# Kernel tuning notes

Measured on AMD Instinct MI355X. Metric: run time of the kernel, lower is better.

Reference implementation:

```python
import jax, jax.numpy as jnp
import numpy as np


def setup_inputs() -> dict:
    key = jax.random.key(0)
    k1, k2, k3 = jax.random.split(key, 3)
    B, H, L, D = 4, 16, 1024, 64
    q = jax.random.normal(k1, (B, H, L, D), dtype=jnp.float32)
    k = jax.random.normal(k2, (B, H, L, D), dtype=jnp.float32)
    attn_mask = jax.random.randint(k3, (B, H, L, L), 0, 2).astype(bool)
    return {"q": q, "k": k, "attn_mask": attn_mask}


def reference(q, k, attn_mask):
    # q, k: [B, H, L, D]. The original builds a [B,H,L,D,L] tensor
    # c[b,h,i,m,j] = exp(-(q[b,h,i,m]-k[b,h,j,m])^2), then for each dim m
    # keeps only the entries where rank of q[i,m] (along seq) equals rank of
    # k[j,m], scatters them into an LxL grid and averages over m.
    # Equivalent fused form: sort q and k per dimension, pair equal ranks,
    # and scatter-add exp(-(q_sorted - k_sorted)^2)/D into p[b,h,i,j].
    B, H, L, D = q.shape
    q_idx = jnp.argsort(q, axis=2)                       # [B,H,L,D] int
    k_idx = jnp.argsort(k, axis=2)
    q_sorted = jnp.take_along_axis(q, q_idx, axis=2)     # [B,H,L,D]
    k_sorted = jnp.take_along_axis(k, k_idx, axis=2)
    diff = q_sorted - k_sorted
    vals = jnp.exp(-(diff * diff))                       # [B,H,L,D]
    # linear index into the flattened [L,L] grid, plus batch*head offset
    lin = q_idx * L + k_idx                              # [B,H,L,D]
    bh_off = (jnp.arange(B * H) * (L * L)).reshape(B, H, 1, 1)
    flat_idx = (lin + bh_off).ravel()
    p = jnp.zeros(B * H * L * L, dtype=q.dtype).at[flat_idx].add(vals.ravel())
    p = (p / D).reshape(B, H, L, L)
    return jnp.where(attn_mask, jnp.zeros((), dtype=p.dtype), p)
```

## Files before the change

kernel.cpp:

```cpp
#include <hip/hip_runtime.h>
#include <stdint.h>
#include <string.h>


#define LL 1024
#define DD 64
#define NBH 64
#define PAIRS_BYTES ((size_t)NBH * DD * LL * 4)

typedef float    vf4   __attribute__((ext_vector_type(4)));
typedef uint32_t vu4   __attribute__((ext_vector_type(4)));
typedef int32_t  vi4   __attribute__((ext_vector_type(4)));

__device__ __forceinline__ uint32_t f2ord(float x) {
    uint32_t u = __float_as_uint(x);
    return (u & 0x80000000u) ? ~u : (u | 0x80000000u);
}
__device__ __forceinline__ float ord2f(uint32_t o) {
    uint32_t u = (o & 0x80000000u) ? (o & 0x7fffffffu) : ~o;
    return __uint_as_float(u);
}
__device__ __forceinline__ void cex(uint64_t& a, uint64_t& b, bool up) {
    const uint64_t lo = a < b ? a : b;
    const uint64_t hi = a < b ? b : a;
    a = up ? lo : hi; b = up ? hi : lo;
}
__device__ __forceinline__ uint64_t shfl64(uint64_t v, int m) {
    const uint32_t lo = __shfl_xor((uint32_t)v, m);
    const uint32_t hi = __shfl_xor((uint32_t)(v >> 32), m);
    return ((uint64_t)hi << 32) | lo;
}

__device__ __forceinline__ void wave_bitonic16(uint64_t x[16], const int lane) {
    #pragma unroll
    for (int lk = 1; lk <= 3; ++lk) {
        const int k2 = 1 << lk;
        #pragma unroll
        for (int j = k2 >> 1; j >= 1; j >>= 1) {
            #pragma unroll
            for (int s = 0; s < 16; ++s)
                if ((s & j) == 0) cex(x[s], x[s | j], ((s & k2) == 0));
        }
    }
    {
        const bool up = ((lane & 1) == 0);
        #pragma unroll
        for (int j = 8; j >= 1; j >>= 1) {
            #pragma unroll
            for (int s = 0; s < 16; ++s)
                if ((s & j) == 0) cex(x[s], x[s | j], up);
        }
    }
    #pragma unroll
    for (int lk = 5; lk <= 10; ++lk) {
        const bool up = ((lane & (1 << (lk - 4))) == 0);
        #pragma unroll
        for (int m = 1 << (lk - 5); m >= 1; m >>= 1) {
            const bool keepmin = (((lane & m) == 0) == up);
            #pragma unroll
            for (int s = 0; s < 16; ++s) {
                const uint64_t y = shfl64(x[s], m);
                x[s] = keepmin ? (x[s] < y ? x[s] : y)
                               : (x[s] > y ? x[s] : y);
            }
        }
        #pragma unroll
        for (int j = 8; j >= 1; j >>= 1) {
            #pragma unroll
            for (int s = 0; s < 16; ++s)
                if ((s & j) == 0) cex(x[s], x[s | j], up);
        }
    }
}

__global__ __launch_bounds__(256, 3) void swd3_phase1(
    const float* __restrict__ q, const float* __restrict__ k,
    uint32_t* __restrict__ pairs)
{
    __shared__ alignas(16) uint32_t pr[4][LL];

    const int raw  = blockIdx.x;
    const int slot = raw >> 3;
    const int bh   = (raw & 7) * 8 + (slot >> 4);
    const int dg   = slot & 15;
    const int t    = threadIdx.x;
    const int w    = t >> 6;
    const int lane = t & 63;
    const int d    = dg * 4 + w;

    const size_t colbase = (size_t)bh * (LL * DD) + d;

    uint64_t xq[16], xk[16];
    #pragma unroll
    for (int s = 0; s < 16; ++s) {
        const uint32_t e = 16u * (uint32_t)lane + (uint32_t)s;
        xq[s] = ((uint64_t)f2ord(q[colbase + (size_t)e * DD]) << 32) | e;
        xk[s] = ((uint64_t)f2ord(k[colbase + (size_t)e * DD]) << 32) | e;
    }
    wave_bitonic16(xq, lane);
    wave_bitonic16(xk, lane);

    uint32_t* prw = pr[w];
    #pragma unroll
    for (int s = 0; s < 16; ++s) {
        const uint32_t iq = (uint32_t)xq[s] & 1023u;
        const uint32_t ik = (uint32_t)xk[s] & 1023u;
        const float df = ord2f((uint32_t)(xq[s] >> 32))
                       - ord2f((uint32_t)(xk[s] >> 32));
        const float val = __expf(-df * df) * (1.0f / 64.0f);
        prw[iq] = (__float_as_uint(val) & 0xFFFFFC00u) | ik;
    }
    __asm__ volatile("s_waitcnt lgkmcnt(0)" ::: "memory");
    vu4* pp4 = (vu4*)(pairs + ((size_t)bh * DD + d) * LL);
    const vu4* src = (const vu4*)prw;
    #pragma unroll
    for (int r = 0; r < 4; ++r)
        pp4[r * 64 + lane] = src[r * 64 + lane];
}

__global__ __launch_bounds__(256) void swd3_phase2(
    const uint32_t* __restrict__ pairs, const void* __restrict__ maskp,
    float* __restrict__ out)
{
    __shared__ alignas(16) float acc[8 * LL];
    __shared__ uint32_t sdet[4];

    const int bh = blockIdx.x >> 7;
    const int s  = blockIdx.x & 127;
    const int i0 = s * 8;
    const int t  = threadIdx.x;

    {
        const uint32_t w = ((const uint32_t*)maskp)[t];
        const uint64_t bal = __ballot(w > 1u);
        if ((t & 63) == 0) sdet[t >> 6] = (bal != 0ull) ? 1u : 0u;
    }

    vf4* acc4 = (vf4*)acc;
    #pragma unroll
    for (int v = 0; v < 8; ++v) {
        vf4 z; z.x = 0.f; z.y = 0.f; z.z = 0.f; z.w = 0.f;
        acc4[v * 256 + t] = z;
    }
    __syncthreads();

    const bool mask_byte =
        ((sdet[0] | sdet[1] | sdet[2] | sdet[3]) != 0u);
    const size_t cellbase = ((size_t)bh << 20) + ((size_t)i0 << 10);

    uint32_t mb[8];
    vi4      mi[8];
    if (mask_byte) {
        const uint32_t* mp = (const uint32_t*)maskp + (cellbase >> 2);
        #pragma unroll
        for (int v = 0; v < 8; ++v)
            mb[v] = __builtin_nontemporal_load(mp + v * 256 + t);
    } else {
        const vi4* mp = (const vi4*)((const int32_t*)maskp + cellbase);
        #pragma unroll
        for (int v = 0; v < 8; ++v)
            mi[v] = __builtin_nontemporal_load(mp + v * 256 + t);
    }

    {
        const uint32_t* pb = pairs + (size_t)bh * (DD * LL);
        const int dd = t >> 2;
        const uint2 pv = ((const uint2*)(pb + dd * LL + i0))[t & 3];
        const int ii0 = 2 * (t & 3), ii1 = ii0 + 1;
        atomicAdd(&acc[ii0 * LL + (int)(pv.x & 1023u)],
                  __uint_as_float(pv.x & 0xFFFFFC00u));
        atomicAdd(&acc[ii1 * LL + (int)(pv.y & 1023u)],
                  __uint_as_float(pv.y & 0xFFFFFC00u));
    }
    __syncthreads();

    vf4* ob = (vf4*)(out + cellbase);
    #pragma unroll
    for (int v = 0; v < 8; ++v) {
        const int p = v * 256 + t;
        const vf4 a = acc4[p];
        int mx, my, mz, mw2;
        if (mask_byte) {
            const uint32_t m = mb[v];
            mx = (int)(m & 0xFFu); my = (int)((m >> 8) & 0xFFu);
            mz = (int)((m >> 16) & 0xFFu); mw2 = (int)(m >> 24);
        } else {
            mx = mi[v].x; my = mi[v].y; mz = mi[v].z; mw2 = mi[v].w;
        }
        vf4 r;
        r.x = mx  ? 0.f : a.x;
        r.y = my  ? 0.f : a.y;
        r.z = mz  ? 0.f : a.z;
        r.w = mw2 ? 0.f : a.w;
        __builtin_nontemporal_store(r, ob + p);
    }
}

extern "C" void kernel_launch(void* const* d_in, const int* in_sizes, int n_in,
                              void* d_out, int out_size, void* d_ws, size_t ws_size,
                              hipStream_t stream) {
    const float* q = (const float*)d_in[0];
    const float* k = (const float*)d_in[1];
    const void* mask = d_in[2];
    uint32_t* pairs = (uint32_t*)d_ws;

    const bool ws_ok = (ws_size >= PAIRS_BYTES);
    hipError_t e1 = hipSuccess, e2 = hipSuccess;
    (void)hipGetLastError();

    if (ws_ok) {
        swd3_phase1<<<NBH * DD / 4, 256, 0, stream>>>(q, k, pairs);
        swd3_phase1<<<NBH * DD / 4, 256, 0, stream>>>(q, k, pairs);
        e1 = hipGetLastError();
        swd3_phase2<<<NBH * 128, 256, 0, stream>>>(pairs, mask, (float*)d_out);
        e2 = hipGetLastError();
    }

    if (!ws_ok || e1 != hipSuccess || e2 != hipSuccess) {
        static float h_stamp[8];
        h_stamp[0] = !ws_ok ? (9000.0f + (float)(ws_size >> 20))
                            : (1000.0f + (float)(int)e1);
        h_stamp[1] = 2000.0f + (float)(int)e2;
        h_stamp[2] = h_stamp[0];
        h_stamp[3] = h_stamp[1];
        hipMemcpyAsync(d_out, h_stamp, sizeof(h_stamp),
                       hipMemcpyHostToDevice, stream);
    }
}
```

Before: 634.9 us.

## Pre-transpose q/k into column-major workspace and drop the duplicate sort launch

Adds a tiled shared-memory transpose kernel that writes q and k as order-preserving uint32 keys in a per-dimension contiguous layout. This lets the sort kernel read each column with coalesced 16-byte vector loads instead of 256-byte-strided scalar loads. The redundant second launch of the sort kernel is removed. The block index of the scatter/mask kernel is also swizzled to interleave batch-heads. The cost is an extra kernel launch, an extra pass over q and k, and a workspace three times larger; if the workspace is too small, the error-stamp fallback runs instead of the computation.

```diff
diff --git a/kernel.cpp b/kernel.cpp
--- a/kernel.cpp
+++ b/kernel.cpp
@@ -6,7 +6,8 @@
 #define LL 1024
 #define DD 64
 #define NBH 64
-#define PAIRS_BYTES ((size_t)NBH * DD * LL * 4)
+#define MAT_WORDS ((size_t)NBH * DD * LL)
+#define WS_BYTES (3 * MAT_WORDS * 4)
 
 typedef float    vf4   __attribute__((ext_vector_type(4)));
 typedef uint32_t vu4   __attribute__((ext_vector_type(4)));
@@ -73,8 +74,49 @@
     }
 }
 
+__global__ __launch_bounds__(256) void swd3_transpose(
+    const float* __restrict__ q, const float* __restrict__ k,
+    uint32_t* __restrict__ qt, uint32_t* __restrict__ kt)
+{
+    __shared__ uint32_t tq[64][65];
+    __shared__ uint32_t tk[64][65];
+
+    const int b  = blockIdx.x;
+    const int bh = (b & 7) * 8 + ((b >> 3) & 7);
+    const int e0 = (b >> 6) * 64;
+    const int t  = threadIdx.x;
+
+    const size_t base = (size_t)bh * (LL * DD);
+    #pragma unroll
+    for (int i = 0; i < 4; ++i) {
+        const int idx = i * 256 + t;
+        const int r   = idx >> 4;
+        const int c   = (idx & 15) * 4;
+        const vf4 vq = *(const vf4*)(q + base + (size_t)(e0 + r) * DD + c);
+        const vf4 vk = *(const vf4*)(k + base + (size_t)(e0 + r) * DD + c);
+        tq[r][c + 0] = f2ord(vq.x); tq[r][c + 1] = f2ord(vq.y);
+        tq[r][c + 2] = f2ord(vq.z); tq[r][c + 3] = f2ord(vq.w);
+        tk[r][c + 0] = f2ord(vk.x); tk[r][c + 1] = f2ord(vk.y);
+        tk[r][c + 2] = f2ord(vk.z); tk[r][c + 3] = f2ord(vk.w);
+    }
+    __syncthreads();
+    #pragma unroll
+    for (int i = 0; i < 4; ++i) {
+        const int idx = i * 256 + t;
+        const int d   = idx >> 4;
+        const int c   = (idx & 15) * 4;
+        vu4 v;
+        v.x = tq[c + 0][d]; v.y = tq[c + 1][d];
+        v.z = tq[c + 2][d]; v.w = tq[c + 3][d];
+        *(vu4*)(qt + base + (size_t)d * LL + e0 + c) = v;
+        v.x = tk[c + 0][d]; v.y = tk[c + 1][d];
+        v.z = tk[c + 2][d]; v.w = tk[c + 3][d];
+        *(vu4*)(kt + base + (size_t)d * LL + e0 + c) = v;
+    }
+}
+
 __global__ __launch_bounds__(256, 3) void swd3_phase1(
-    const float* __restrict__ q, const float* __restrict__ k,
+    const uint32_t* __restrict__ qt, const uint32_t* __restrict__ kt,
     uint32_t* __restrict__ pairs)
 {
     __shared__ alignas(16) uint32_t pr[4][LL];
@@ -88,14 +130,23 @@
     const int lane = t & 63;
     const int d    = dg * 4 + w;
 
-    const size_t colbase = (size_t)bh * (LL * DD) + d;
+    const uint32_t* colq = qt + (size_t)bh * (DD * LL) + (size_t)d * LL;
+    const uint32_t* colk = kt + (size_t)bh * (DD * LL) + (size_t)d * LL;
 
     uint64_t xq[16], xk[16];
     #pragma unroll
-    for (int s = 0; s < 16; ++s) {
-        const uint32_t e = 16u * (uint32_t)lane + (uint32_t)s;
-        xq[s] = ((uint64_t)f2ord(q[colbase + (size_t)e * DD]) << 32) | e;
-        xk[s] = ((uint64_t)f2ord(k[colbase + (size_t)e * DD]) << 32) | e;
+    for (int r = 0; r < 4; ++r) {
+        const vu4 vq = *(const vu4*)(colq + 256 * r + 4 * lane);
+        const vu4 vk = *(const vu4*)(colk + 256 * r + 4 * lane);
+        const uint32_t eb = 256u * r + 4u * lane;
+        xq[4 * r + 0] = ((uint64_t)vq.x << 32) | (eb + 0);
+        xq[4 * r + 1] = ((uint64_t)vq.y << 32) | (eb + 1);
+        xq[4 * r + 2] = ((uint64_t)vq.z << 32) | (eb + 2);
+        xq[4 * r + 3] = ((uint64_t)vq.w << 32) | (eb + 3);
+        xk[4 * r + 0] = ((uint64_t)vk.x << 32) | (eb + 0);
+        xk[4 * r + 1] = ((uint64_t)vk.y << 32) | (eb + 1);
+        xk[4 * r + 2] = ((uint64_t)vk.z << 32) | (eb + 2);
+        xk[4 * r + 3] = ((uint64_t)vk.w << 32) | (eb + 3);
     }
     wave_bitonic16(xq, lane);
     wave_bitonic16(xk, lane);
@@ -125,9 +176,10 @@
     __shared__ alignas(16) float acc[8 * LL];
     __shared__ uint32_t sdet[4];
 
-    const int bh = blockIdx.x >> 7;
-    const int s  = blockIdx.x & 127;
-    const int i0 = s * 8;
+    const int b  = blockIdx.x;
+    const int bh = (b & 7) * 8 + ((b >> 3) & 7);
+    const int st = b >> 6;
+    const int i0 = st * 8;
     const int t  = threadIdx.x;
 
     {
@@ -203,26 +255,29 @@
     const float* k = (const float*)d_in[1];
     const void* mask = d_in[2];
     uint32_t* pairs = (uint32_t*)d_ws;
-
-    const bool ws_ok = (ws_size >= PAIRS_BYTES);
-    hipError_t e1 = hipSuccess, e2 = hipSuccess;
+    uint32_t* qt = pairs + MAT_WORDS;
+    uint32_t* kt = qt + MAT_WORDS;
+
+    const bool ws_ok = (ws_size >= WS_BYTES);
+    hipError_t e0 = hipSuccess, e1 = hipSuccess, e2 = hipSuccess;
     (void)hipGetLastError();
 
     if (ws_ok) {
-        swd3_phase1<<<NBH * DD / 4, 256, 0, stream>>>(q, k, pairs);
-        swd3_phase1<<<NBH * DD / 4, 256, 0, stream>>>(q, k, pairs);
+        swd3_transpose<<<NBH * 16, 256, 0, stream>>>(q, k, qt, kt);
+        e0 = hipGetLastError();
+        swd3_phase1<<<NBH * DD / 4, 256, 0, stream>>>(qt, kt, pairs);
         e1 = hipGetLastError();
         swd3_phase2<<<NBH * 128, 256, 0, stream>>>(pairs, mask, (float*)d_out);
         e2 = hipGetLastError();
     }
 
-    if (!ws_ok || e1 != hipSuccess || e2 != hipSuccess) {
+    if (!ws_ok || e0 != hipSuccess || e1 != hipSuccess || e2 != hipSuccess) {
         static float h_stamp[8];
         h_stamp[0] = !ws_ok ? (9000.0f + (float)(ws_size >> 20))
-                            : (1000.0f + (float)(int)e1);
-        h_stamp[1] = 2000.0f + (float)(int)e2;
-        h_stamp[2] = h_stamp[0];
-        h_stamp[3] = h_stamp[1];
+                            : (1000.0f + (float)(int)e0);
+        h_stamp[1] = 2000.0f + (float)(int)e1;
+        h_stamp[2] = 3000.0f + (float)(int)e2;
+        h_stamp[3] = h_stamp[0];
         hipMemcpyAsync(d_out, h_stamp, sizeof(h_stamp),
                        hipMemcpyHostToDevice, stream);
     }
```

Measured after the change: 551.8 us. 1.15x faster.
